# Performance work log

Measured on AMD Instinct MI355X. Metric: run time of the kernel, lower is better.

The kernel has to match this reference:

```python
import jax, jax.numpy as jnp
import numpy as np

IN_SIZE = 256    # network input size
N_NODES = 1024   # hidden+output nodes, processed in topological order
DEG = 32         # fixed fan-in per node
BATCH = 16384
OUT_SIZE = 16    # last OUT_SIZE nodes are output nodes (is_output=True)


def setup_inputs() -> dict:
    key = jax.random.key(0)
    kx, kw = jax.random.split(key)
    x = jax.random.normal(kx, (BATCH, IN_SIZE), dtype=jnp.float32)
    weights = jax.random.normal(kw, (N_NODES, DEG), dtype=jnp.float32)
    # node i may only read network inputs and outputs of nodes < i
    rng = np.random.default_rng(0)
    in_idxs = np.stack([rng.integers(0, IN_SIZE + i, size=DEG) for i in range(N_NODES)])
    return {"x": x, "weights": weights, "in_idxs": jnp.asarray(in_idxs, dtype=jnp.int32)}


def reference(x, weights, in_idxs):
    B = x.shape[0]
    # activs buffer: [B, in_size + n_nodes + 1], inputs written to front
    activs = jnp.zeros((B, IN_SIZE + N_NODES + 1), dtype=x.dtype)
    activs = activs.at[:, :IN_SIZE].set(x)
    write_pos = IN_SIZE + jnp.arange(N_NODES, dtype=jnp.int32)

    def step(a, node):
        idxs, w, pos = node
        gathered = jnp.take(a, idxs, axis=1)      # [B, DEG]  index_select
        n_out = jnp.tanh(gathered @ w)            # [B]       matmul + activation
        a = a.at[:, pos].set(n_out)               # sequential write into buffer
        return a, n_out

    _, outs = jax.lax.scan(step, activs, (in_idxs, weights, write_pos))
    # output nodes are the last OUT_SIZE nodes; torch.tensor(out) stacks -> [OUT_SIZE, B]
    return outs[-OUT_SIZE:]
```

## Files before the change

### kernel.cpp

```cpp
#include <hip/hip_runtime.h>

#define IN_SIZE 256
#define N_NODES 1024
#define DEG 32
#define BATCH 16384
#define OUT_SIZE 16
#define COLS 4
#define N_ROWS (IN_SIZE + N_NODES)
#define NPAIR (N_NODES / 2)

__device__ __forceinline__ unsigned short f2bf_rne(float f) {
    const unsigned u = __float_as_uint(f);
    return (unsigned short)((u + 0x7FFFu + ((u >> 16) & 1u)) >> 16);
}

__device__ __forceinline__ float tanh6(float z) {
    const float s = __expf(-2.0f * fabsf(z));
    const float r = __builtin_amdgcn_rcpf(1.0f + s);
    return copysignf(fmaf(-s, r, r), z);
}

template <int CTRL>
__device__ __forceinline__ float dpp_add(float v) {
    return v + __int_as_float(__builtin_amdgcn_mov_dpp(__float_as_int(v), CTRL, 0xF, 0xF, true));
}
__device__ __forceinline__ float dpp_ror8(float v) {
    return __int_as_float(__builtin_amdgcn_mov_dpp(__float_as_int(v), 0x128, 0xF, 0xF, true));
}

__global__ __launch_bounds__(64) void ne_detect(const void* __restrict__ xraw,
                                                int* __restrict__ flag) {
    const unsigned short* xb = (const unsigned short*)xraw;
    const int tid = threadIdx.x;
    int plausible = 0;
    for (int k = tid; k < 2048; k += 64) {
        const float v = __uint_as_float((unsigned)xb[2 * k] << 16);
        const float a = fabsf(v);
        plausible += (a == 0.0f) || (a > 1e-3f && a < 1e3f) ? 1 : 0;
    }
    for (int off = 32; off > 0; off >>= 1) plausible += __shfl_down(plausible, off);
    if (tid == 0) *flag = (plausible >= (2048 * 9) / 10) ? 1 : 0;
}

__global__ __launch_bounds__(256) void ne_prep(const void* __restrict__ wraw,
                                               const int* __restrict__ idxs,
                                               int4* __restrict__ pki,
                                               float4* __restrict__ pkw,
                                               float4* __restrict__ hza,
                                               float* __restrict__ hcc,
                                               const int* __restrict__ flag) {
    const int isbf16 = *flag;
    const int tid = blockIdx.x * 256 + threadIdx.x;
    const int stride = gridDim.x * 256;
    const unsigned short* wb = (const unsigned short*)wraw;
    const float* wsrc = (const float*)wraw;
    for (int k = tid; k < N_NODES * 8; k += stride) {
        const int n = k >> 3, qq = k & 7;
        const int e = n * DEG + qq * 4;
        pki[k] = make_int4(idxs[e], idxs[e + 1], idxs[e + 2], idxs[e + 3]);
        float w0 = isbf16 ? __uint_as_float((unsigned)wb[e + 0] << 16) : wsrc[e + 0];
        float w1 = isbf16 ? __uint_as_float((unsigned)wb[e + 1] << 16) : wsrc[e + 1];
        float w2 = isbf16 ? __uint_as_float((unsigned)wb[e + 2] << 16) : wsrc[e + 2];
        float w3 = isbf16 ? __uint_as_float((unsigned)wb[e + 3] << 16) : wsrc[e + 3];
        pkw[k] = make_float4(w0, w1, w2, w3);
    }
    for (int n = tid; n < N_NODES; n += stride) {
        float h1 = 0.f, h2 = 0.f, h3 = 0.f, h4 = 0.f, h5 = 0.f;
        for (int r = 0; r < DEG; ++r) {
            const int id = idxs[n * DEG + r];
            if (id < IN_SIZE) continue;
            const int d = IN_SIZE + n - id;
            if (d < 1 || d > 5) continue;
            const float w = isbf16 ? __uint_as_float((unsigned)wb[n * DEG + r] << 16)
                                   : wsrc[n * DEG + r];
            if (d == 1) h1 += w; else if (d == 2) h2 += w; else if (d == 3) h3 += w;
            else if (d == 4) h4 += w; else h5 += w;
        }
        const float4 a = (n & 1) ? make_float4(h2, h3, h4, h5)
                                 : make_float4(h2, h1, h4, h3);
        const float hc = (n & 1) ? h1 : 0.0f;
#pragma unroll
        for (int r = 0; r < 8; ++r) { hza[n * 8 + r] = a; hcc[n * 8 + r] = hc; }
    }
}

__global__ __launch_bounds__(64) void ne_forward(const void* __restrict__ xraw,
                                                 const int4* __restrict__ pki,
                                                 const float4* __restrict__ pkw,
                                                 const float4* __restrict__ hza,
                                                 const float* __restrict__ hcc,
                                                 void* __restrict__ outraw,
                                                 const int* __restrict__ flag) {
    __shared__ float act[N_ROWS * COLS];
    const int lane = threadIdx.x;
    const int q = lane & 7;
    const int h = (lane >> 3) & 1;
    const int c = lane >> 4;
    const int l15 = lane & 15;
    const int c0 = blockIdx.x * COLS;
    const int isbf16 = *flag;
    float* outf = (float*)outraw;
    unsigned short* outb = (unsigned short*)outraw;

    {
        float4* az = (float4*)(act + IN_SIZE * COLS);
#pragma unroll
        for (int t = 0; t < 16; ++t) az[t * 64 + lane] = make_float4(0.f, 0.f, 0.f, 0.f);
    }
    {
        const int b = c;
        if (isbf16) {
            const unsigned short* xb =
                (const unsigned short*)xraw + (size_t)(c0 + b) * IN_SIZE + l15 * 16;
#pragma unroll
            for (int t = 0; t < 2; ++t) {
                const uint4 v = *(const uint4*)(xb + t * 8);
                const int k0 = l15 * 16 + t * 8;
                act[(k0 + 0) * COLS + b] = __uint_as_float(v.x << 16);
                act[(k0 + 1) * COLS + b] = __uint_as_float(v.x & 0xFFFF0000u);
                act[(k0 + 2) * COLS + b] = __uint_as_float(v.y << 16);
                act[(k0 + 3) * COLS + b] = __uint_as_float(v.y & 0xFFFF0000u);
                act[(k0 + 4) * COLS + b] = __uint_as_float(v.z << 16);
                act[(k0 + 5) * COLS + b] = __uint_as_float(v.z & 0xFFFF0000u);
                act[(k0 + 6) * COLS + b] = __uint_as_float(v.w << 16);
                act[(k0 + 7) * COLS + b] = __uint_as_float(v.w & 0xFFFF0000u);
            }
        } else {
            const float* xs = (const float*)xraw + (size_t)(c0 + b) * IN_SIZE + l15 * 16;
#pragma unroll
            for (int t = 0; t < 4; ++t) {
                const float4 v = *(const float4*)(xs + t * 4);
                const int k0 = l15 * 16 + t * 4;
                act[(k0 + 0) * COLS + b] = v.x;
                act[(k0 + 1) * COLS + b] = v.y;
                act[(k0 + 2) * COLS + b] = v.z;
                act[(k0 + 3) * COLS + b] = v.w;
            }
        }
    }

    float accA, accB;
    float gA0, gA1, gA2, gA3, gB0, gB1, gB2, gB3;
    {
        const int4 it = pki[(0 << 4) + l15];
        const float4 wt = pkw[(0 << 4) + l15];
        const float x0 = act[it.x * COLS + c], x1 = act[it.y * COLS + c];
        const float x2 = act[it.z * COLS + c], x3 = act[it.w * COLS + c];
        float zr = x0 * wt.x; zr = fmaf(x1, wt.y, zr);
        zr = fmaf(x2, wt.z, zr); zr = fmaf(x3, wt.w, zr);
        zr = dpp_add<0xB1>(zr); zr = dpp_add<0x4E>(zr); zr = dpp_add<0x141>(zr);
        accA = zr;
    }
    {
        const int4 it = pki[(1 << 4) + l15];
        gA0 = act[it.x * COLS + c]; gA1 = act[it.y * COLS + c];
        gA2 = act[it.z * COLS + c]; gA3 = act[it.w * COLS + c];
    }
    int4   idv0 = pki[(2 << 4) + l15], idv1 = pki[(3 << 4) + l15];
    float4 wv0  = pkw[(1 << 4) + l15], wv1  = pkw[(2 << 4) + l15];
    float4 hza0 = hza[(0 << 4) + l15], hza1 = hza[(1 << 4) + l15];
    float  hcc0 = hcc[(0 << 4) + l15], hcc1 = hcc[(1 << 4) + l15];
    float tsP1 = 0.f, toP1 = 0.f, tsP2 = 0.f, toP2 = 0.f;

#define PAIRSTEP(S, GC0, GC1, GC2, GC3, GN0, GN1, GN2, GN3,                            \
                 IDV, WVV, HZA, HCC, ACCc, ACCn, OUT, CLAMP)                           \
    {                                                                                  \
                                      \
        float zr = GC0 * WVV.x; zr = fmaf(GC1, WVV.y, zr);                             \
        zr = fmaf(GC2, WVV.z, zr); zr = fmaf(GC3, WVV.w, zr);                          \
        zr = dpp_add<0xB1>(zr); zr = dpp_add<0x4E>(zr); zr = dpp_add<0x141>(zr);       \
        ACCn = zr;                                                                     \
                \
        GN0 = act[IDV.x * COLS + c]; GN1 = act[IDV.y * COLS + c];                      \
        GN2 = act[IDV.z * COLS + c]; GN3 = act[IDV.w * COLS + c];                      \
                                                               \
        float z = fmaf(HZA.x, tsP1, ACCc);                                             \
        z = fmaf(HZA.y, toP1, z);                                                      \
        z = fmaf(HZA.z, tsP2, z);                                                      \
        z = fmaf(HZA.w, toP2, z);                                                      \
        const float t1 = tanh6(z);                                                     \
        z = fmaf(HCC, dpp_ror8(t1), z);                  \
        const float t = tanh6(z);                                                      \
        if (q == 0) {                                                                  \
            act[(IN_SIZE + 2 * (S) + h) * COLS + c] = t;                               \
            if (OUT) {                                                                 \
                const size_t o =                                                       \
                    (size_t)(2 * (S) + h - (N_NODES - OUT_SIZE)) * BATCH + c0 + c;     \
                if (isbf16) outb[o] = f2bf_rne(t); else outf[o] = t;                   \
            }                                                                          \
        }                                                                              \
        tsP2 = tsP1; toP2 = toP1; tsP1 = t; toP1 = dpp_ror8(t);                        \
                      \
        { const int Pw = (CLAMP) ? (((S) + 3 < NPAIR) ? (S) + 3 : NPAIR - 1) : (S) + 3;\
          const int Pn = (CLAMP) ? (((S) + 4 < NPAIR) ? (S) + 4 : NPAIR - 1) : (S) + 4;\
          const int Ph = (CLAMP) ? (((S) + 2 < NPAIR) ? (S) + 2 : NPAIR - 1) : (S) + 2;\
          WVV = pkw[(Pw << 4) + l15];                                                  \
          IDV = pki[(Pn << 4) + l15];                                                  \
          HZA = hza[(Ph << 4) + l15];                                                  \
          HCC = hcc[(Ph << 4) + l15]; }                                                \
    }

#pragma unroll 1
    for (int S = 0; S < NPAIR - 8; S += 2) {
        PAIRSTEP(S,     gA0, gA1, gA2, gA3, gB0, gB1, gB2, gB3,
                 idv0, wv0, hza0, hcc0, accA, accB, 0, 0)
        PAIRSTEP(S + 1, gB0, gB1, gB2, gB3, gA0, gA1, gA2, gA3,
                 idv1, wv1, hza1, hcc1, accB, accA, 0, 0)
    }
    {
        const int S = NPAIR - 8;
        PAIRSTEP(S + 0, gA0, gA1, gA2, gA3, gB0, gB1, gB2, gB3,
                 idv0, wv0, hza0, hcc0, accA, accB, 1, 1)
        PAIRSTEP(S + 1, gB0, gB1, gB2, gB3, gA0, gA1, gA2, gA3,
                 idv1, wv1, hza1, hcc1, accB, accA, 1, 1)
        PAIRSTEP(S + 2, gA0, gA1, gA2, gA3, gB0, gB1, gB2, gB3,
                 idv0, wv0, hza0, hcc0, accA, accB, 1, 1)
        PAIRSTEP(S + 3, gB0, gB1, gB2, gB3, gA0, gA1, gA2, gA3,
                 idv1, wv1, hza1, hcc1, accB, accA, 1, 1)
        PAIRSTEP(S + 4, gA0, gA1, gA2, gA3, gB0, gB1, gB2, gB3,
                 idv0, wv0, hza0, hcc0, accA, accB, 1, 1)
        PAIRSTEP(S + 5, gB0, gB1, gB2, gB3, gA0, gA1, gA2, gA3,
                 idv1, wv1, hza1, hcc1, accB, accA, 1, 1)
        PAIRSTEP(S + 6, gA0, gA1, gA2, gA3, gB0, gB1, gB2, gB3,
                 idv0, wv0, hza0, hcc0, accA, accB, 1, 1)
        PAIRSTEP(S + 7, gB0, gB1, gB2, gB3, gA0, gA1, gA2, gA3,
                 idv1, wv1, hza1, hcc1, accB, accA, 1, 1)
    }
#undef PAIRSTEP
}

extern "C" void kernel_launch(void* const* d_in, const int* in_sizes, int n_in,
                              void* d_out, int out_size, void* d_ws, size_t ws_size,
                              hipStream_t stream) {
    const void* x   = d_in[0];
    const void* w   = d_in[1];
    const int* idxs = (const int*)d_in[2];

    int4*   pki = (int4*)d_ws;
    float4* pkw = (float4*)((char*)d_ws + (size_t)128 * 1024);
    float4* hza = (float4*)((char*)d_ws + (size_t)256 * 1024);
    float*  hcc = (float*)((char*)d_ws + (size_t)384 * 1024);
    int* flag   = (int*)((char*)d_ws + ((ws_size - 16) & ~(size_t)15));

    ne_detect<<<1, 64, 0, stream>>>(x, flag);
    ne_prep<<<32, 256, 0, stream>>>(w, idxs, pki, pkw, hza, hcc, flag);

    ne_forward<<<dim3(BATCH / COLS), dim3(64), 0, stream>>>(x, pki, pkw, hza, hcc,
                                                            d_out, flag);
}
```

Before: 291.4 us.

## Process both nodes of a pair per lane group and double batch columns per block

Each 8-lane group now handles one batch column and computes both the even and odd node of a pair, instead of splitting the pair across two 8-lane halves and exchanging values with DPP row rotates. COLS doubles to 8, so each wave covers 8 batch columns and the grid halves. The prep kernel interleaves even/odd index and weight packs and splits the near-dependency correction coefficients into separate even/odd arrays. This removes the cross-half DPP exchanges and doubles the work per wave, at the cost of twice the shared memory per block (40KB), more registers per lane and a longer serial chain per step.

```diff
diff --git a/kernel.cpp b/kernel.cpp
--- a/kernel.cpp
+++ b/kernel.cpp
@@ -5,7 +5,7 @@
 #define DEG 32
 #define BATCH 16384
 #define OUT_SIZE 16
-#define COLS 4
+#define COLS 8
 #define N_ROWS (IN_SIZE + N_NODES)
 #define NPAIR (N_NODES / 2)
 
@@ -23,9 +23,6 @@
 template <int CTRL>
 __device__ __forceinline__ float dpp_add(float v) {
     return v + __int_as_float(__builtin_amdgcn_mov_dpp(__float_as_int(v), CTRL, 0xF, 0xF, true));
-}
-__device__ __forceinline__ float dpp_ror8(float v) {
-    return __int_as_float(__builtin_amdgcn_mov_dpp(__float_as_int(v), 0x128, 0xF, 0xF, true));
 }
 
 __global__ __launch_bounds__(64) void ne_detect(const void* __restrict__ xraw,
@@ -46,8 +43,9 @@
                                                const int* __restrict__ idxs,
                                                int4* __restrict__ pki,
                                                float4* __restrict__ pkw,
-                                               float4* __restrict__ hza,
-                                               float* __restrict__ hcc,
+                                               float4* __restrict__ hze4,
+                                               float4* __restrict__ hzo4,
+                                               float* __restrict__ h1o,
                                                const int* __restrict__ flag) {
     const int isbf16 = *flag;
     const int tid = blockIdx.x * 256 + threadIdx.x;
@@ -57,12 +55,13 @@
     for (int k = tid; k < N_NODES * 8; k += stride) {
         const int n = k >> 3, qq = k & 7;
         const int e = n * DEG + qq * 4;
-        pki[k] = make_int4(idxs[e], idxs[e + 1], idxs[e + 2], idxs[e + 3]);
+        const int dest = (n >> 1) * 16 + qq * 2 + (n & 1);
+        pki[dest] = make_int4(idxs[e], idxs[e + 1], idxs[e + 2], idxs[e + 3]);
         float w0 = isbf16 ? __uint_as_float((unsigned)wb[e + 0] << 16) : wsrc[e + 0];
         float w1 = isbf16 ? __uint_as_float((unsigned)wb[e + 1] << 16) : wsrc[e + 1];
         float w2 = isbf16 ? __uint_as_float((unsigned)wb[e + 2] << 16) : wsrc[e + 2];
         float w3 = isbf16 ? __uint_as_float((unsigned)wb[e + 3] << 16) : wsrc[e + 3];
-        pkw[k] = make_float4(w0, w1, w2, w3);
+        pkw[dest] = make_float4(w0, w1, w2, w3);
     }
     for (int n = tid; n < N_NODES; n += stride) {
         float h1 = 0.f, h2 = 0.f, h3 = 0.f, h4 = 0.f, h5 = 0.f;
@@ -76,28 +75,34 @@
             if (d == 1) h1 += w; else if (d == 2) h2 += w; else if (d == 3) h3 += w;
             else if (d == 4) h4 += w; else h5 += w;
         }
-        const float4 a = (n & 1) ? make_float4(h2, h3, h4, h5)
-                                 : make_float4(h2, h1, h4, h3);
-        const float hc = (n & 1) ? h1 : 0.0f;
-#pragma unroll
-        for (int r = 0; r < 8; ++r) { hza[n * 8 + r] = a; hcc[n * 8 + r] = hc; }
+        const int P = n >> 1;
+        if ((n & 1) == 0) {
+#pragma unroll
+            for (int r = 0; r < 8; ++r) hze4[P * 8 + r] = make_float4(h1, h2, h3, h4);
+        } else {
+#pragma unroll
+            for (int r = 0; r < 8; ++r) {
+                hzo4[P * 8 + r] = make_float4(h2, h3, h4, h5);
+                h1o[P * 8 + r] = h1;
+            }
+        }
     }
 }
 
 __global__ __launch_bounds__(64) void ne_forward(const void* __restrict__ xraw,
                                                  const int4* __restrict__ pki,
                                                  const float4* __restrict__ pkw,
-                                                 const float4* __restrict__ hza,
-                                                 const float* __restrict__ hcc,
+                                                 const float4* __restrict__ hze4,
+                                                 const float4* __restrict__ hzo4,
+                                                 const float* __restrict__ h1o,
                                                  void* __restrict__ outraw,
                                                  const int* __restrict__ flag) {
     __shared__ float act[N_ROWS * COLS];
     const int lane = threadIdx.x;
     const int q = lane & 7;
-    const int h = (lane >> 3) & 1;
-    const int c = lane >> 4;
-    const int l15 = lane & 15;
+    const int c = lane >> 3;
     const int c0 = blockIdx.x * COLS;
+    const int q2 = q * 2;
     const int isbf16 = *flag;
     float* outf = (float*)outraw;
     unsigned short* outb = (unsigned short*)outraw;
@@ -105,17 +110,18 @@
     {
         float4* az = (float4*)(act + IN_SIZE * COLS);
 #pragma unroll
-        for (int t = 0; t < 16; ++t) az[t * 64 + lane] = make_float4(0.f, 0.f, 0.f, 0.f);
-    }
-    {
-        const int b = c;
+        for (int t = 0; t < 32; ++t) az[t * 64 + lane] = make_float4(0.f, 0.f, 0.f, 0.f);
+    }
+    {
+        const int b = lane >> 3;
+        const int seg = lane & 7;
         if (isbf16) {
             const unsigned short* xb =
-                (const unsigned short*)xraw + (size_t)(c0 + b) * IN_SIZE + l15 * 16;
-#pragma unroll
-            for (int t = 0; t < 2; ++t) {
+                (const unsigned short*)xraw + (size_t)(c0 + b) * IN_SIZE + seg * 32;
+#pragma unroll
+            for (int t = 0; t < 4; ++t) {
                 const uint4 v = *(const uint4*)(xb + t * 8);
-                const int k0 = l15 * 16 + t * 8;
+                const int k0 = seg * 32 + t * 8;
                 act[(k0 + 0) * COLS + b] = __uint_as_float(v.x << 16);
                 act[(k0 + 1) * COLS + b] = __uint_as_float(v.x & 0xFFFF0000u);
                 act[(k0 + 2) * COLS + b] = __uint_as_float(v.y << 16);
@@ -126,11 +132,11 @@
                 act[(k0 + 7) * COLS + b] = __uint_as_float(v.w & 0xFFFF0000u);
             }
         } else {
-            const float* xs = (const float*)xraw + (size_t)(c0 + b) * IN_SIZE + l15 * 16;
-#pragma unroll
-            for (int t = 0; t < 4; ++t) {
+            const float* xs = (const float*)xraw + (size_t)(c0 + b) * IN_SIZE + seg * 32;
+#pragma unroll
+            for (int t = 0; t < 8; ++t) {
                 const float4 v = *(const float4*)(xs + t * 4);
-                const int k0 = l15 * 16 + t * 4;
+                const int k0 = seg * 32 + t * 4;
                 act[(k0 + 0) * COLS + b] = v.x;
                 act[(k0 + 1) * COLS + b] = v.y;
                 act[(k0 + 2) * COLS + b] = v.z;
@@ -139,92 +145,96 @@
         }
     }
 
-    float accA, accB;
-    float gA0, gA1, gA2, gA3, gB0, gB1, gB2, gB3;
-    {
-        const int4 it = pki[(0 << 4) + l15];
-        const float4 wt = pkw[(0 << 4) + l15];
-        const float x0 = act[it.x * COLS + c], x1 = act[it.y * COLS + c];
-        const float x2 = act[it.z * COLS + c], x3 = act[it.w * COLS + c];
-        float zr = x0 * wt.x; zr = fmaf(x1, wt.y, zr);
-        zr = fmaf(x2, wt.z, zr); zr = fmaf(x3, wt.w, zr);
-        zr = dpp_add<0xB1>(zr); zr = dpp_add<0x4E>(zr); zr = dpp_add<0x141>(zr);
-        accA = zr;
-    }
-    {
-        const int4 it = pki[(1 << 4) + l15];
-        gA0 = act[it.x * COLS + c]; gA1 = act[it.y * COLS + c];
-        gA2 = act[it.z * COLS + c]; gA3 = act[it.w * COLS + c];
-    }
-    int4   idv0 = pki[(2 << 4) + l15], idv1 = pki[(3 << 4) + l15];
-    float4 wv0  = pkw[(1 << 4) + l15], wv1  = pkw[(2 << 4) + l15];
-    float4 hza0 = hza[(0 << 4) + l15], hza1 = hza[(1 << 4) + l15];
-    float  hcc0 = hcc[(0 << 4) + l15], hcc1 = hcc[(1 << 4) + l15];
-    float tsP1 = 0.f, toP1 = 0.f, tsP2 = 0.f, toP2 = 0.f;
-
-#define PAIRSTEP(S, GC0, GC1, GC2, GC3, GN0, GN1, GN2, GN3,                            \
-                 IDV, WVV, HZA, HCC, ACCc, ACCn, OUT, CLAMP)                           \
+    float zeA, zoA, zeB, zoB;
+    float gE0, gE1, gE2, gE3, gO0, gO1, gO2, gO3;
+    {
+        const int4 iE = pki[0 * 16 + q2], iO = pki[0 * 16 + q2 + 1];
+        const float4 wE = pkw[0 * 16 + q2], wO = pkw[0 * 16 + q2 + 1];
+        float ze = act[iE.x * COLS + c] * wE.x;
+        ze = fmaf(act[iE.y * COLS + c], wE.y, ze);
+        ze = fmaf(act[iE.z * COLS + c], wE.z, ze);
+        ze = fmaf(act[iE.w * COLS + c], wE.w, ze);
+        float zo = act[iO.x * COLS + c] * wO.x;
+        zo = fmaf(act[iO.y * COLS + c], wO.y, zo);
+        zo = fmaf(act[iO.z * COLS + c], wO.z, zo);
+        zo = fmaf(act[iO.w * COLS + c], wO.w, zo);
+        ze = dpp_add<0xB1>(ze); ze = dpp_add<0x4E>(ze); ze = dpp_add<0x141>(ze);
+        zo = dpp_add<0xB1>(zo); zo = dpp_add<0x4E>(zo); zo = dpp_add<0x141>(zo);
+        zeA = ze; zoA = zo;
+    }
+    {
+        const int4 iE = pki[1 * 16 + q2], iO = pki[1 * 16 + q2 + 1];
+        gE0 = act[iE.x * COLS + c]; gE1 = act[iE.y * COLS + c];
+        gE2 = act[iE.z * COLS + c]; gE3 = act[iE.w * COLS + c];
+        gO0 = act[iO.x * COLS + c]; gO1 = act[iO.y * COLS + c];
+        gO2 = act[iO.z * COLS + c]; gO3 = act[iO.w * COLS + c];
+    }
+    int4   idE0 = pki[2 * 16 + q2], idO0 = pki[2 * 16 + q2 + 1];
+    int4   idE1 = pki[3 * 16 + q2], idO1 = pki[3 * 16 + q2 + 1];
+    float4 wvE0 = pkw[1 * 16 + q2], wvO0 = pkw[1 * 16 + q2 + 1];
+    float4 wvE1 = pkw[2 * 16 + q2], wvO1 = pkw[2 * 16 + q2 + 1];
+    float4 heA = hze4[0 * 8 + q], hoA = hzo4[0 * 8 + q];
+    float4 heB = hze4[1 * 8 + q], hoB = hzo4[1 * 8 + q];
+    float  c1A = h1o[0 * 8 + q],  c1B = h1o[1 * 8 + q];
+    float te1 = 0.f, to1 = 0.f, te2 = 0.f, to2 = 0.f;
+
+#define PAIRSTEP(S, IDE, IDO, WVE, WVO, HZE, HZO, H1, ZEc, ZOc, ZEn, ZOn, OUT, CLAMP)  \
     {                                                                                  \
                                       \
-        float zr = GC0 * WVV.x; zr = fmaf(GC1, WVV.y, zr);                             \
-        zr = fmaf(GC2, WVV.z, zr); zr = fmaf(GC3, WVV.w, zr);                          \
-        zr = dpp_add<0xB1>(zr); zr = dpp_add<0x4E>(zr); zr = dpp_add<0x141>(zr);       \
-        ACCn = zr;                                                                     \
-                \
-        GN0 = act[IDV.x * COLS + c]; GN1 = act[IDV.y * COLS + c];                      \
-        GN2 = act[IDV.z * COLS + c]; GN3 = act[IDV.w * COLS + c];                      \
+        float ze = gE0 * WVE.x; ze = fmaf(gE1, WVE.y, ze);                             \
+        ze = fmaf(gE2, WVE.z, ze); ze = fmaf(gE3, WVE.w, ze);                          \
+        float zo = gO0 * WVO.x; zo = fmaf(gO1, WVO.y, zo);                             \
+        zo = fmaf(gO2, WVO.z, zo); zo = fmaf(gO3, WVO.w, zo);                          \
+        ze = dpp_add<0xB1>(ze); ze = dpp_add<0x4E>(ze); ze = dpp_add<0x141>(ze);       \
+        zo = dpp_add<0xB1>(zo); zo = dpp_add<0x4E>(zo); zo = dpp_add<0x141>(zo);       \
+        ZEn = ze; ZOn = zo;                                                            \
+                   \
+        gE0 = act[IDE.x * COLS + c]; gE1 = act[IDE.y * COLS + c];                      \
+        gE2 = act[IDE.z * COLS + c]; gE3 = act[IDE.w * COLS + c];                      \
+        gO0 = act[IDO.x * COLS + c]; gO1 = act[IDO.y * COLS + c];                      \
+        gO2 = act[IDO.z * COLS + c]; gO3 = act[IDO.w * COLS + c];                      \
                                                                \
-        float z = fmaf(HZA.x, tsP1, ACCc);                                             \
-        z = fmaf(HZA.y, toP1, z);                                                      \
-        z = fmaf(HZA.z, tsP2, z);                                                      \
-        z = fmaf(HZA.w, toP2, z);                                                      \
-        const float t1 = tanh6(z);                                                     \
-        z = fmaf(HCC, dpp_ror8(t1), z);                  \
-        const float t = tanh6(z);                                                      \
-        if (q == 0) {                                                                  \
-            act[(IN_SIZE + 2 * (S) + h) * COLS + c] = t;                               \
+        float zE = fmaf(HZE.x, to1, ZEc); zE = fmaf(HZE.y, te1, zE);                   \
+        zE = fmaf(HZE.z, to2, zE); zE = fmaf(HZE.w, te2, zE);                          \
+        float zO = fmaf(HZO.x, to1, ZOc); zO = fmaf(HZO.y, te1, zO);                   \
+        zO = fmaf(HZO.z, to2, zO); zO = fmaf(HZO.w, te2, zO);                          \
+        const float te = tanh6(zE);                                                    \
+        zO = fmaf(H1, te, zO);                                                         \
+        const float to = tanh6(zO);                                                    \
+        if (q < 2) {                                                                   \
+            act[(IN_SIZE + 2 * (S) + q) * COLS + c] = q ? to : te;                     \
             if (OUT) {                                                                 \
                 const size_t o =                                                       \
-                    (size_t)(2 * (S) + h - (N_NODES - OUT_SIZE)) * BATCH + c0 + c;     \
-                if (isbf16) outb[o] = f2bf_rne(t); else outf[o] = t;                   \
+                    (size_t)(2 * (S) + q - (N_NODES - OUT_SIZE)) * BATCH + c0 + c;     \
+                if (isbf16) outb[o] = f2bf_rne(q ? to : te);                           \
+                else        outf[o] = q ? to : te;                                     \
             }                                                                          \
         }                                                                              \
-        tsP2 = tsP1; toP2 = toP1; tsP1 = t; toP1 = dpp_ror8(t);                        \
-                      \
+        te2 = te1; to2 = to1; te1 = te; to1 = to;                                      \
+                                            \
         { const int Pw = (CLAMP) ? (((S) + 3 < NPAIR) ? (S) + 3 : NPAIR - 1) : (S) + 3;\
           const int Pn = (CLAMP) ? (((S) + 4 < NPAIR) ? (S) + 4 : NPAIR - 1) : (S) + 4;\
           const int Ph = (CLAMP) ? (((S) + 2 < NPAIR) ? (S) + 2 : NPAIR - 1) : (S) + 2;\
-          WVV = pkw[(Pw << 4) + l15];                                                  \
-          IDV = pki[(Pn << 4) + l15];                                                  \
-          HZA = hza[(Ph << 4) + l15];                                                  \
-          HCC = hcc[(Ph << 4) + l15]; }                                                \
+          WVE = pkw[Pw * 16 + q2]; WVO = pkw[Pw * 16 + q2 + 1];                        \
+          IDE = pki[Pn * 16 + q2]; IDO = pki[Pn * 16 + q2 + 1];                        \
+          HZE = hze4[Ph * 8 + q]; HZO = hzo4[Ph * 8 + q]; H1 = h1o[Ph * 8 + q]; }      \
     }
 
 #pragma unroll 1
     for (int S = 0; S < NPAIR - 8; S += 2) {
-        PAIRSTEP(S,     gA0, gA1, gA2, gA3, gB0, gB1, gB2, gB3,
-                 idv0, wv0, hza0, hcc0, accA, accB, 0, 0)
-        PAIRSTEP(S + 1, gB0, gB1, gB2, gB3, gA0, gA1, gA2, gA3,
-                 idv1, wv1, hza1, hcc1, accB, accA, 0, 0)
+        PAIRSTEP(S,     idE0, idO0, wvE0, wvO0, heA, hoA, c1A, zeA, zoA, zeB, zoB, 0, 0)
+        PAIRSTEP(S + 1, idE1, idO1, wvE1, wvO1, heB, hoB, c1B, zeB, zoB, zeA, zoA, 0, 0)
     }
     {
         const int S = NPAIR - 8;
-        PAIRSTEP(S + 0, gA0, gA1, gA2, gA3, gB0, gB1, gB2, gB3,
-                 idv0, wv0, hza0, hcc0, accA, accB, 1, 1)
-        PAIRSTEP(S + 1, gB0, gB1, gB2, gB3, gA0, gA1, gA2, gA3,
-                 idv1, wv1, hza1, hcc1, accB, accA, 1, 1)
-        PAIRSTEP(S + 2, gA0, gA1, gA2, gA3, gB0, gB1, gB2, gB3,
-                 idv0, wv0, hza0, hcc0, accA, accB, 1, 1)
-        PAIRSTEP(S + 3, gB0, gB1, gB2, gB3, gA0, gA1, gA2, gA3,
-                 idv1, wv1, hza1, hcc1, accB, accA, 1, 1)
-        PAIRSTEP(S + 4, gA0, gA1, gA2, gA3, gB0, gB1, gB2, gB3,
-                 idv0, wv0, hza0, hcc0, accA, accB, 1, 1)
-        PAIRSTEP(S + 5, gB0, gB1, gB2, gB3, gA0, gA1, gA2, gA3,
-                 idv1, wv1, hza1, hcc1, accB, accA, 1, 1)
-        PAIRSTEP(S + 6, gA0, gA1, gA2, gA3, gB0, gB1, gB2, gB3,
-                 idv0, wv0, hza0, hcc0, accA, accB, 1, 1)
-        PAIRSTEP(S + 7, gB0, gB1, gB2, gB3, gA0, gA1, gA2, gA3,
-                 idv1, wv1, hza1, hcc1, accB, accA, 1, 1)
+        PAIRSTEP(S + 0, idE0, idO0, wvE0, wvO0, heA, hoA, c1A, zeA, zoA, zeB, zoB, 1, 1)
+        PAIRSTEP(S + 1, idE1, idO1, wvE1, wvO1, heB, hoB, c1B, zeB, zoB, zeA, zoA, 1, 1)
+        PAIRSTEP(S + 2, idE0, idO0, wvE0, wvO0, heA, hoA, c1A, zeA, zoA, zeB, zoB, 1, 1)
+        PAIRSTEP(S + 3, idE1, idO1, wvE1, wvO1, heB, hoB, c1B, zeB, zoB, zeA, zoA, 1, 1)
+        PAIRSTEP(S + 4, idE0, idO0, wvE0, wvO0, heA, hoA, c1A, zeA, zoA, zeB, zoB, 1, 1)
+        PAIRSTEP(S + 5, idE1, idO1, wvE1, wvO1, heB, hoB, c1B, zeB, zoB, zeA, zoA, 1, 1)
+        PAIRSTEP(S + 6, idE0, idO0, wvE0, wvO0, heA, hoA, c1A, zeA, zoA, zeB, zoB, 1, 1)
+        PAIRSTEP(S + 7, idE1, idO1, wvE1, wvO1, heB, hoB, c1B, zeB, zoB, zeA, zoA, 1, 1)
     }
 #undef PAIRSTEP
 }
@@ -236,15 +246,16 @@
     const void* w   = d_in[1];
     const int* idxs = (const int*)d_in[2];
 
-    int4*   pki = (int4*)d_ws;
-    float4* pkw = (float4*)((char*)d_ws + (size_t)128 * 1024);
-    float4* hza = (float4*)((char*)d_ws + (size_t)256 * 1024);
-    float*  hcc = (float*)((char*)d_ws + (size_t)384 * 1024);
-    int* flag   = (int*)((char*)d_ws + ((ws_size - 16) & ~(size_t)15));
+    int4*   pki  = (int4*)d_ws;
+    float4* pkw  = (float4*)((char*)d_ws + (size_t)128 * 1024);
+    float4* hze4 = (float4*)((char*)d_ws + (size_t)256 * 1024);
+    float4* hzo4 = (float4*)((char*)d_ws + (size_t)320 * 1024);
+    float*  h1o  = (float*)((char*)d_ws + (size_t)384 * 1024);
+    int* flag    = (int*)((char*)d_ws + ((ws_size - 16) & ~(size_t)15));
 
     ne_detect<<<1, 64, 0, stream>>>(x, flag);
-    ne_prep<<<32, 256, 0, stream>>>(w, idxs, pki, pkw, hza, hcc, flag);
-
-    ne_forward<<<dim3(BATCH / COLS), dim3(64), 0, stream>>>(x, pki, pkw, hza, hcc,
-                                                            d_out, flag);
-}
+    ne_prep<<<32, 256, 0, stream>>>(w, idxs, pki, pkw, hze4, hzo4, h1o, flag);
+
+    ne_forward<<<dim3(BATCH / COLS), dim3(64), 0, stream>>>(x, pki, pkw, hze4, hzo4,
+                                                            h1o, d_out, flag);
+}
```

After: 304.6 us. +4.5%, slower.

## Deepen gather prefetch and extend recent-node bypass to distance seven

Applied to the files above, without the earlier changes.

The shared-memory gather for each node pair now starts one pair earlier, which gives LDS loads more time to complete. To keep that safe, the register bypass for recently computed activations is widened from distance 5 to distance 7, adding two FMA terms per step. Indices are also pre-scaled to byte offsets in the prep kernel, which removes the address multiply in the inner loop. The cost is more registers and FMAs on the serial dependency chain.

```diff
diff --git a/kernel.cpp b/kernel.cpp
--- a/kernel.cpp
+++ b/kernel.cpp
@@ -46,8 +46,8 @@
                                                const int* __restrict__ idxs,
                                                int4* __restrict__ pki,
                                                float4* __restrict__ pkw,
-                                               float4* __restrict__ hza,
-                                               float* __restrict__ hcc,
+                                               float4* __restrict__ hzA,
+                                               float4* __restrict__ hzB,
                                                const int* __restrict__ flag) {
     const int isbf16 = *flag;
     const int tid = blockIdx.x * 256 + threadIdx.x;
@@ -57,7 +57,8 @@
     for (int k = tid; k < N_NODES * 8; k += stride) {
         const int n = k >> 3, qq = k & 7;
         const int e = n * DEG + qq * 4;
-        pki[k] = make_int4(idxs[e], idxs[e + 1], idxs[e + 2], idxs[e + 3]);
+        pki[k] = make_int4(idxs[e] * 16, idxs[e + 1] * 16,
+                           idxs[e + 2] * 16, idxs[e + 3] * 16);
         float w0 = isbf16 ? __uint_as_float((unsigned)wb[e + 0] << 16) : wsrc[e + 0];
         float w1 = isbf16 ? __uint_as_float((unsigned)wb[e + 1] << 16) : wsrc[e + 1];
         float w2 = isbf16 ? __uint_as_float((unsigned)wb[e + 2] << 16) : wsrc[e + 2];
@@ -65,30 +66,30 @@
         pkw[k] = make_float4(w0, w1, w2, w3);
     }
     for (int n = tid; n < N_NODES; n += stride) {
-        float h1 = 0.f, h2 = 0.f, h3 = 0.f, h4 = 0.f, h5 = 0.f;
+        float h[8] = {0.f, 0.f, 0.f, 0.f, 0.f, 0.f, 0.f, 0.f};
         for (int r = 0; r < DEG; ++r) {
             const int id = idxs[n * DEG + r];
             if (id < IN_SIZE) continue;
             const int d = IN_SIZE + n - id;
-            if (d < 1 || d > 5) continue;
+            if (d < 1 || d > 7) continue;
             const float w = isbf16 ? __uint_as_float((unsigned)wb[n * DEG + r] << 16)
                                    : wsrc[n * DEG + r];
-            if (d == 1) h1 += w; else if (d == 2) h2 += w; else if (d == 3) h3 += w;
-            else if (d == 4) h4 += w; else h5 += w;
+            h[d] += w;
         }
-        const float4 a = (n & 1) ? make_float4(h2, h3, h4, h5)
-                                 : make_float4(h2, h1, h4, h3);
-        const float hc = (n & 1) ? h1 : 0.0f;
-#pragma unroll
-        for (int r = 0; r < 8; ++r) { hza[n * 8 + r] = a; hcc[n * 8 + r] = hc; }
+        const float4 a = (n & 1) ? make_float4(h[2], h[3], h[4], h[5])
+                                 : make_float4(h[2], h[1], h[4], h[3]);
+        const float4 b = (n & 1) ? make_float4(h[6], h[7], h[1], 0.f)
+                                 : make_float4(h[6], h[5], 0.f, 0.f);
+#pragma unroll
+        for (int r = 0; r < 8; ++r) { hzA[n * 8 + r] = a; hzB[n * 8 + r] = b; }
     }
 }
 
 __global__ __launch_bounds__(64) void ne_forward(const void* __restrict__ xraw,
                                                  const int4* __restrict__ pki,
                                                  const float4* __restrict__ pkw,
-                                                 const float4* __restrict__ hza,
-                                                 const float* __restrict__ hcc,
+                                                 const float4* __restrict__ hzA,
+                                                 const float4* __restrict__ hzB,
                                                  void* __restrict__ outraw,
                                                  const int* __restrict__ flag) {
     __shared__ float act[N_ROWS * COLS];
@@ -97,8 +98,10 @@
     const int h = (lane >> 3) & 1;
     const int c = lane >> 4;
     const int l15 = lane & 15;
+    const int c4 = c * 4;
     const int c0 = blockIdx.x * COLS;
     const int isbf16 = *flag;
+    const char* actb = (const char*)act;
     float* outf = (float*)outraw;
     unsigned short* outb = (unsigned short*)outraw;
 
@@ -142,44 +145,54 @@
     float accA, accB;
     float gA0, gA1, gA2, gA3, gB0, gB1, gB2, gB3;
     {
-        const int4 it = pki[(0 << 4) + l15];
-        const float4 wt = pkw[(0 << 4) + l15];
-        const float x0 = act[it.x * COLS + c], x1 = act[it.y * COLS + c];
-        const float x2 = act[it.z * COLS + c], x3 = act[it.w * COLS + c];
-        float zr = x0 * wt.x; zr = fmaf(x1, wt.y, zr);
-        zr = fmaf(x2, wt.z, zr); zr = fmaf(x3, wt.w, zr);
+        const int4 it = pki[0 * 16 + l15];
+        const float4 wt = pkw[0 * 16 + l15];
+        float zr =      *(const float*)(actb + (unsigned)(it.x + c4)) * wt.x;
+        zr = fmaf(*(const float*)(actb + (unsigned)(it.y + c4)), wt.y, zr);
+        zr = fmaf(*(const float*)(actb + (unsigned)(it.z + c4)), wt.z, zr);
+        zr = fmaf(*(const float*)(actb + (unsigned)(it.w + c4)), wt.w, zr);
         zr = dpp_add<0xB1>(zr); zr = dpp_add<0x4E>(zr); zr = dpp_add<0x141>(zr);
         accA = zr;
     }
     {
-        const int4 it = pki[(1 << 4) + l15];
-        gA0 = act[it.x * COLS + c]; gA1 = act[it.y * COLS + c];
-        gA2 = act[it.z * COLS + c]; gA3 = act[it.w * COLS + c];
-    }
-    int4   idv0 = pki[(2 << 4) + l15], idv1 = pki[(3 << 4) + l15];
-    float4 wv0  = pkw[(1 << 4) + l15], wv1  = pkw[(2 << 4) + l15];
-    float4 hza0 = hza[(0 << 4) + l15], hza1 = hza[(1 << 4) + l15];
-    float  hcc0 = hcc[(0 << 4) + l15], hcc1 = hcc[(1 << 4) + l15];
-    float tsP1 = 0.f, toP1 = 0.f, tsP2 = 0.f, toP2 = 0.f;
-
-#define PAIRSTEP(S, GC0, GC1, GC2, GC3, GN0, GN1, GN2, GN3,                            \
-                 IDV, WVV, HZA, HCC, ACCc, ACCn, OUT, CLAMP)                           \
+        const int4 i1 = pki[1 * 16 + l15];
+        gA0 = *(const float*)(actb + (unsigned)(i1.x + c4));
+        gA1 = *(const float*)(actb + (unsigned)(i1.y + c4));
+        gA2 = *(const float*)(actb + (unsigned)(i1.z + c4));
+        gA3 = *(const float*)(actb + (unsigned)(i1.w + c4));
+        const int4 i2 = pki[2 * 16 + l15];
+        gB0 = *(const float*)(actb + (unsigned)(i2.x + c4));
+        gB1 = *(const float*)(actb + (unsigned)(i2.y + c4));
+        gB2 = *(const float*)(actb + (unsigned)(i2.z + c4));
+        gB3 = *(const float*)(actb + (unsigned)(i2.w + c4));
+    }
+    int4   idv0 = pki[3 * 16 + l15], idv1 = pki[4 * 16 + l15];
+    float4 wv0  = pkw[1 * 16 + l15], wv1  = pkw[2 * 16 + l15];
+    float4 hA0 = hzA[0 * 16 + l15], hB0 = hzB[0 * 16 + l15];
+    float4 hA1 = hzA[1 * 16 + l15], hB1 = hzB[1 * 16 + l15];
+    float ts1 = 0.f, to1 = 0.f, ts2 = 0.f, to2 = 0.f, ts3 = 0.f, to3 = 0.f;
+
+#define PAIRSTEP(S, GC0, GC1, GC2, GC3, IDV, WVV, HA, HB, ACCc, ACCn, OUT, CLAMP)      \
     {                                                                                  \
                                       \
         float zr = GC0 * WVV.x; zr = fmaf(GC1, WVV.y, zr);                             \
         zr = fmaf(GC2, WVV.z, zr); zr = fmaf(GC3, WVV.w, zr);                          \
         zr = dpp_add<0xB1>(zr); zr = dpp_add<0x4E>(zr); zr = dpp_add<0x141>(zr);       \
         ACCn = zr;                                                                     \
-                \
-        GN0 = act[IDV.x * COLS + c]; GN1 = act[IDV.y * COLS + c];                      \
-        GN2 = act[IDV.z * COLS + c]; GN3 = act[IDV.w * COLS + c];                      \
+                    \
+        GC0 = *(const float*)(actb + (unsigned)(IDV.x + c4));                          \
+        GC1 = *(const float*)(actb + (unsigned)(IDV.y + c4));                          \
+        GC2 = *(const float*)(actb + (unsigned)(IDV.z + c4));                          \
+        GC3 = *(const float*)(actb + (unsigned)(IDV.w + c4));                          \
                                                                \
-        float z = fmaf(HZA.x, tsP1, ACCc);                                             \
-        z = fmaf(HZA.y, toP1, z);                                                      \
-        z = fmaf(HZA.z, tsP2, z);                                                      \
-        z = fmaf(HZA.w, toP2, z);                                                      \
+        float z = fmaf(HA.x, ts1, ACCc);                                               \
+        z = fmaf(HA.y, to1, z);                                                        \
+        z = fmaf(HA.z, ts2, z);                                                        \
+        z = fmaf(HA.w, to2, z);                                                        \
+        z = fmaf(HB.x, ts3, z);                                                        \
+        z = fmaf(HB.y, to3, z);                                                        \
         const float t1 = tanh6(z);                                                     \
-        z = fmaf(HCC, dpp_ror8(t1), z);                  \
+        z = fmaf(HB.z, dpp_ror8(t1), z);               \
         const float t = tanh6(z);                                                      \
         if (q == 0) {                                                                  \
             act[(IN_SIZE + 2 * (S) + h) * COLS + c] = t;                               \
@@ -189,42 +202,33 @@
                 if (isbf16) outb[o] = f2bf_rne(t); else outf[o] = t;                   \
             }                                                                          \
         }                                                                              \
-        tsP2 = tsP1; toP2 = toP1; tsP1 = t; toP1 = dpp_ror8(t);                        \
+        ts3 = ts2; to3 = to2; ts2 = ts1; to2 = to1;                                    \
+        ts1 = t; to1 = dpp_ror8(t);                                                    \
                       \
         { const int Pw = (CLAMP) ? (((S) + 3 < NPAIR) ? (S) + 3 : NPAIR - 1) : (S) + 3;\
-          const int Pn = (CLAMP) ? (((S) + 4 < NPAIR) ? (S) + 4 : NPAIR - 1) : (S) + 4;\
+          const int Pn = (CLAMP) ? (((S) + 5 < NPAIR) ? (S) + 5 : NPAIR - 1) : (S) + 5;\
           const int Ph = (CLAMP) ? (((S) + 2 < NPAIR) ? (S) + 2 : NPAIR - 1) : (S) + 2;\
           WVV = pkw[(Pw << 4) + l15];                                                  \
           IDV = pki[(Pn << 4) + l15];                                                  \
-          HZA = hza[(Ph << 4) + l15];                                                  \
-          HCC = hcc[(Ph << 4) + l15]; }                                                \
+          HA  = hzA[(Ph << 4) + l15];                                                  \
+          HB  = hzB[(Ph << 4) + l15]; }                                                \
     }
 
 #pragma unroll 1
     for (int S = 0; S < NPAIR - 8; S += 2) {
-        PAIRSTEP(S,     gA0, gA1, gA2, gA3, gB0, gB1, gB2, gB3,
-                 idv0, wv0, hza0, hcc0, accA, accB, 0, 0)
-        PAIRSTEP(S + 1, gB0, gB1, gB2, gB3, gA0, gA1, gA2, gA3,
-                 idv1, wv1, hza1, hcc1, accB, accA, 0, 0)
+        PAIRSTEP(S,     gA0, gA1, gA2, gA3, idv0, wv0, hA0, hB0, accA, accB, 0, 0)
+        PAIRSTEP(S + 1, gB0, gB1, gB2, gB3, idv1, wv1, hA1, hB1, accB, accA, 0, 0)
     }
     {
         const int S = NPAIR - 8;
-        PAIRSTEP(S + 0, gA0, gA1, gA2, gA3, gB0, gB1, gB2, gB3,
-                 idv0, wv0, hza0, hcc0, accA, accB, 1, 1)
-        PAIRSTEP(S + 1, gB0, gB1, gB2, gB3, gA0, gA1, gA2, gA3,
-                 idv1, wv1, hza1, hcc1, accB, accA, 1, 1)
-        PAIRSTEP(S + 2, gA0, gA1, gA2, gA3, gB0, gB1, gB2, gB3,
-                 idv0, wv0, hza0, hcc0, accA, accB, 1, 1)
-        PAIRSTEP(S + 3, gB0, gB1, gB2, gB3, gA0, gA1, gA2, gA3,
-                 idv1, wv1, hza1, hcc1, accB, accA, 1, 1)
-        PAIRSTEP(S + 4, gA0, gA1, gA2, gA3, gB0, gB1, gB2, gB3,
-                 idv0, wv0, hza0, hcc0, accA, accB, 1, 1)
-        PAIRSTEP(S + 5, gB0, gB1, gB2, gB3, gA0, gA1, gA2, gA3,
-                 idv1, wv1, hza1, hcc1, accB, accA, 1, 1)
-        PAIRSTEP(S + 6, gA0, gA1, gA2, gA3, gB0, gB1, gB2, gB3,
-                 idv0, wv0, hza0, hcc0, accA, accB, 1, 1)
-        PAIRSTEP(S + 7, gB0, gB1, gB2, gB3, gA0, gA1, gA2, gA3,
-                 idv1, wv1, hza1, hcc1, accB, accA, 1, 1)
+        PAIRSTEP(S + 0, gA0, gA1, gA2, gA3, idv0, wv0, hA0, hB0, accA, accB, 1, 1)
+        PAIRSTEP(S + 1, gB0, gB1, gB2, gB3, idv1, wv1, hA1, hB1, accB, accA, 1, 1)
+        PAIRSTEP(S + 2, gA0, gA1, gA2, gA3, idv0, wv0, hA0, hB0, accA, accB, 1, 1)
+        PAIRSTEP(S + 3, gB0, gB1, gB2, gB3, idv1, wv1, hA1, hB1, accB, accA, 1, 1)
+        PAIRSTEP(S + 4, gA0, gA1, gA2, gA3, idv0, wv0, hA0, hB0, accA, accB, 1, 1)
+        PAIRSTEP(S + 5, gB0, gB1, gB2, gB3, idv1, wv1, hA1, hB1, accB, accA, 1, 1)
+        PAIRSTEP(S + 6, gA0, gA1, gA2, gA3, idv0, wv0, hA0, hB0, accA, accB, 1, 1)
+        PAIRSTEP(S + 7, gB0, gB1, gB2, gB3, idv1, wv1, hA1, hB1, accB, accA, 1, 1)
     }
 #undef PAIRSTEP
 }
@@ -238,13 +242,13 @@
 
     int4*   pki = (int4*)d_ws;
     float4* pkw = (float4*)((char*)d_ws + (size_t)128 * 1024);
-    float4* hza = (float4*)((char*)d_ws + (size_t)256 * 1024);
-    float*  hcc = (float*)((char*)d_ws + (size_t)384 * 1024);
+    float4* hzA = (float4*)((char*)d_ws + (size_t)256 * 1024);
+    float4* hzB = (float4*)((char*)d_ws + (size_t)384 * 1024);
     int* flag   = (int*)((char*)d_ws + ((ws_size - 16) & ~(size_t)15));
 
     ne_detect<<<1, 64, 0, stream>>>(x, flag);
-    ne_prep<<<32, 256, 0, stream>>>(w, idxs, pki, pkw, hza, hcc, flag);
-
-    ne_forward<<<dim3(BATCH / COLS), dim3(64), 0, stream>>>(x, pki, pkw, hza, hcc,
+    ne_prep<<<32, 256, 0, stream>>>(w, idxs, pki, pkw, hzA, hzB, flag);
+
+    ne_forward<<<dim3(BATCH / COLS), dim3(64), 0, stream>>>(x, pki, pkw, hzA, hzB,
                                                             d_out, flag);
 }
```

After: 324.9 us. 1.11x slower.
